# Performance work log

Hardware: AMD Instinct MI355X
Metric: run time of the kernel (lower is better)

The kernel has to match this reference:

```python
import jax, jax.numpy as jnp
import numpy as np
import math

B, T, D = 2, 2048, 2048
H, KV, HD = 16, 4, 128  # n_heads, n_kv_heads, head_dim
ROPE_BASE = 10000.0


def setup_inputs() -> dict:
    key = jax.random.key(0)
    ks = jax.random.split(key, 5)
    s = 0.02
    return {
        "x": jax.random.normal(ks[0], (B, T, D), dtype=jnp.float32),
        "Wq": jax.random.normal(ks[1], (D, H * HD), dtype=jnp.float32) * s,
        "Wk": jax.random.normal(ks[2], (D, KV * HD), dtype=jnp.float32) * s,
        "Wv": jax.random.normal(ks[3], (D, KV * HD), dtype=jnp.float32) * s,
        "Wo": jax.random.normal(ks[4], (H * HD, D), dtype=jnp.float32) * s,
    }


def _rope_tables(t_len, dtype):
    inv_freq = 1.0 / (ROPE_BASE ** (jnp.arange(0, HD, 2, dtype=jnp.float32) / HD))
    t = jnp.arange(t_len, dtype=jnp.float32)
    freqs = t[:, None] * inv_freq[None, :]  # [T, HD/2]
    return jnp.cos(freqs).astype(dtype), jnp.sin(freqs).astype(dtype)


def _apply_rope(x, cos, sin):
    # x: [B, h, T, HD]; cos/sin: [T, HD/2] broadcast to [1,1,T,HD/2]
    c = cos[None, None, :, :]
    s = sin[None, None, :, :]
    x1, x2 = x[..., ::2], x[..., 1::2]
    rot = jnp.stack([x1 * c - x2 * s, x1 * s + x2 * c], axis=-1)  # interleave back
    return rot.reshape(x.shape)


def reference(x, Wq, Wk, Wv, Wo):
    b, t, d = x.shape
    q = (x @ Wq).reshape(b, t, H, HD).transpose(0, 2, 1, 3)   # [B,H,T,HD]
    k = (x @ Wk).reshape(b, t, KV, HD).transpose(0, 2, 1, 3)  # [B,KV,T,HD]
    v = (x @ Wv).reshape(b, t, KV, HD).transpose(0, 2, 1, 3)

    cos, sin = _rope_tables(t, x.dtype)
    q = _apply_rope(q, cos, sin)
    k = _apply_rope(k, cos, sin)

    rep = H // KV
    k_rep = jnp.repeat(k, rep, axis=1)  # [B,H,T,HD]
    v_rep = jnp.repeat(v, rep, axis=1)

    scale = 1.0 / math.sqrt(HD)
    scores = jnp.einsum("bhqd,bhkd->bhqk", q, k_rep) * scale
    causal = jnp.triu(jnp.ones((t, t), dtype=bool), k=1)
    neg = jnp.finfo(scores.dtype).min
    scores = jnp.where(causal[None, None, :, :], neg, scores)
    attn = jax.nn.softmax(scores, axis=-1)
    out = jnp.einsum("bhqk,bhkd->bhqd", attn, v_rep)
    y = out.transpose(0, 2, 1, 3).reshape(b, t, H * HD) @ Wo
    return y
```

## Files before the change

kernel.cpp:

```cpp
#include <hip/hip_runtime.h>
#include <cstdint>
#include <math.h>

#define T_SEQ 2048
#define BATCH 2
#define NH 16
#define NKV 4
#define HD 128

typedef __attribute__((ext_vector_type(8))) short short8;
typedef __attribute__((ext_vector_type(4))) float f32x4;

__device__ __forceinline__ ushort f2bf(float f) {
  uint32_t u = __builtin_bit_cast(uint32_t, f);
  u += 0x7FFF + ((u >> 16) & 1);
  return (ushort)(u >> 16);
}
__device__ __forceinline__ ushort f2bf_trunc(float f) {
  return (ushort)(__builtin_bit_cast(uint32_t, f) >> 16);
}
__device__ __forceinline__ float bf2f(ushort u) {
  uint32_t v = ((uint32_t)u) << 16;
  return __builtin_bit_cast(float, v);
}
__device__ __forceinline__ void ld16(void* lds, const void* g) {
  __builtin_amdgcn_global_load_lds((const __attribute__((address_space(1))) void*)g,
                                   (__attribute__((address_space(3))) void*)lds,
                                   16, 0, 0);
}

__global__ __launch_bounds__(256) void prep(
    const float* __restrict__ x, ushort* __restrict__ xb,
    const float* __restrict__ Wq, const float* __restrict__ Wk,
    const float* __restrict__ Wv, const float* __restrict__ Wo,
    ushort* __restrict__ wqkvT, ushort* __restrict__ woT) {
  __shared__ float tile[32][33];
  const int bid = blockIdx.x;
  const int tid = threadIdx.x;
  if (bid < 8192) {
    int i = (bid * 256 + tid) * 4;
    float4 v = *(const float4*)&x[i];
    ushort4 o;
    o.x = f2bf(v.x); o.y = f2bf(v.y); o.z = f2bf(v.z); o.w = f2bf(v.w);
    *(ushort4*)&xb[i] = o;
    return;
  }
  const float* in;
  ushort* out;
  int N, lid;
  if (bid < 12288)      { in = Wq; out = wqkvT;                        N = 2048; lid = bid - 8192; }
  else if (bid < 13312) { in = Wk; out = wqkvT + (size_t)2048 * 2048;  N = 512;  lid = bid - 12288; }
  else if (bid < 14336) { in = Wv; out = wqkvT + (size_t)2560 * 2048;  N = 512;  lid = bid - 13312; }
  else                  { in = Wo; out = woT;                          N = 2048; lid = bid - 14336; }
  const int K = 2048;
  const int nb = N / 32;
  const int n0 = (lid % nb) * 32, k0 = (lid / nb) * 32;
  const int r = tid >> 3, c4 = (tid & 7) << 2;
  float4 v = *(const float4*)&in[(size_t)(k0 + r) * N + n0 + c4];
  tile[r][c4 + 0] = v.x; tile[r][c4 + 1] = v.y;
  tile[r][c4 + 2] = v.z; tile[r][c4 + 3] = v.w;
  __syncthreads();
  ushort4 o;
  o.x = f2bf(tile[c4 + 0][r]); o.y = f2bf(tile[c4 + 1][r]);
  o.z = f2bf(tile[c4 + 2][r]); o.w = f2bf(tile[c4 + 3][r]);
  *(ushort4*)&out[(size_t)(n0 + r) * K + k0 + c4] = o;
}

template <typename OutT>
__global__ __launch_bounds__(256) void gemm_bt(const ushort* __restrict__ A,
                                               const ushort* __restrict__ Bt,
                                               OutT* __restrict__ C,
                                               int M, int N, int K) {
  __shared__ __align__(16) ushort As[128 * 32];
  __shared__ __align__(16) ushort Bs[128 * 32];
  const int tid = threadIdx.x;
  const int w = tid >> 6, l = tid & 63;
  const int wr = w >> 1, wc = w & 1;
  const int quad = l >> 4, l15 = l & 15;
  const int bm = blockIdx.y * 128, bn = blockIdx.x * 128;

  f32x4 acc[4][4];
#pragma unroll
  for (int mi = 0; mi < 4; ++mi)
#pragma unroll
    for (int ni = 0; ni < 4; ++ni)
#pragma unroll
      for (int r = 0; r < 4; ++r) acc[mi][ni][r] = 0.f;

  for (int k0 = 0; k0 < K; k0 += 32) {
    __syncthreads();
#pragma unroll
    for (int j = 0; j < 2; ++j) {
      int r0 = w * 32 + j * 16;
      int row = r0 + (l >> 2);
      int gc = (l & 3) ^ ((row >> 1) & 3);
      ld16(&As[r0 * 32], &A[(size_t)(bm + row) * K + k0 + gc * 8]);
      ld16(&Bs[r0 * 32], &Bt[(size_t)(bn + row) * K + k0 + gc * 8]);
    }
    __syncthreads();
    short8 af[4], bf[4];
#pragma unroll
    for (int mi = 0; mi < 4; ++mi) {
      int m = wr * 64 + mi * 16 + l15;
      af[mi] = *(const short8*)&As[m * 32 + (quad ^ ((m >> 1) & 3)) * 8];
    }
#pragma unroll
    for (int ni = 0; ni < 4; ++ni) {
      int n = wc * 64 + ni * 16 + l15;
      bf[ni] = *(const short8*)&Bs[n * 32 + (quad ^ ((n >> 1) & 3)) * 8];
    }
#pragma unroll
    for (int mi = 0; mi < 4; ++mi)
#pragma unroll
      for (int ni = 0; ni < 4; ++ni)
        acc[mi][ni] = __builtin_amdgcn_mfma_f32_16x16x32_bf16(af[mi], bf[ni], acc[mi][ni], 0, 0, 0);
  }
#pragma unroll
  for (int mi = 0; mi < 4; ++mi)
#pragma unroll
    for (int ni = 0; ni < 4; ++ni)
#pragma unroll
      for (int r = 0; r < 4; ++r) {
        int grow = bm + wr * 64 + mi * 16 + quad * 4 + r;
        int gcol = bn + wc * 64 + ni * 16 + l15;
        if constexpr (__is_same(OutT, ushort))
          C[(size_t)grow * N + gcol] = f2bf(acc[mi][ni][r]);
        else
          C[(size_t)grow * N + gcol] = acc[mi][ni][r];
      }
}

__global__ __launch_bounds__(256) void rope_k_bf16(ushort* __restrict__ qkv) {
  int idx = blockIdx.x * 256 + threadIdx.x;
  const int PAIRS_PER_ROW = 256;
  if (idx >= BATCH * T_SEQ * PAIRS_PER_ROW) return;
  int row = idx >> 8;
  int kp = idx & 255;
  int t = row & (T_SEQ - 1);
  int i = kp & 63;
  ushort* ptr = qkv + (size_t)row * 3072 + 2048 + 2 * kp;
  float inv = expf((float)i * -0.14391156831212788f);
  float ang = (float)t * inv;
  float sn, cs;
  sincosf(ang, &sn, &cs);
  float x1 = bf2f(ptr[0]), x2 = bf2f(ptr[1]);
  ptr[0] = f2bf(x1 * cs - x2 * sn);
  ptr[1] = f2bf(x1 * sn + x2 * cs);
}

__global__ __launch_bounds__(256) void transpose_v(const ushort* __restrict__ qkv,
                                                   ushort* __restrict__ vT) {
  __shared__ ushort tile[32][34];
  int m0 = blockIdx.x * 32, d0 = blockIdx.y * 32;
  int r = threadIdx.x >> 3, c4 = (threadIdx.x & 7) << 2;
  ushort4 v = *(const ushort4*)&qkv[(size_t)(m0 + r) * 3072 + 2560 + d0 + c4];
  tile[r][c4 + 0] = v.x; tile[r][c4 + 1] = v.y;
  tile[r][c4 + 2] = v.z; tile[r][c4 + 3] = v.w;
  __syncthreads();
  ushort4 o;
  o.x = tile[c4 + 0][r]; o.y = tile[c4 + 1][r];
  o.z = tile[c4 + 2][r]; o.w = tile[c4 + 3][r];
  *(ushort4*)&vT[(size_t)(d0 + r) * 4096 + m0 + c4] = o;
}

__global__ __launch_bounds__(512, 2) void attn_mfma(const ushort* __restrict__ qkv,
                                                    const ushort* __restrict__ vT,
                                                    ushort* __restrict__ ao) {
  __shared__ __align__(16) ushort Ks[2][64 * 128];
  __shared__ __align__(16) ushort Vt[2][128 * 64];
  __shared__ __align__(16) ushort Ps[8][16 * 64];
  const int tid = threadIdx.x;
  const int w = tid >> 6, l = tid & 63;
  const int quad = l >> 4, l15 = l & 15;
  const int hw = w >> 1, sub = w & 1;
  const int kvh = blockIdx.y, b = blockIdx.z;
  const int h = kvh * 4 + hw;
  const size_t krow0 = (size_t)b * T_SEQ;
  const float SC = 0.12751744595764253f;

  ushort* pw = Ps[w];
  const int within = l & 7;
  const int colbase = l15 >> 3;

  auto stage = [&](int kt, int bufi) {
    const int kt0 = kt << 6;
    ushort* kb = Ks[bufi];
    ushort* vb = Vt[bufi];
#pragma unroll
    for (int j = 0; j < 2; ++j) {
      int r0 = w * 8 + j * 4;
      int row = r0 + (l >> 4);
      int gc = (l & 15) ^ ((row >> 1) & 7);
      ld16(&kb[r0 * 128], &qkv[(krow0 + kt0 + row) * 3072 + 2048 + kvh * 128 + gc * 8]);
    }
#pragma unroll
    for (int j = 0; j < 2; ++j) {
      int r0 = w * 16 + j * 8;
      int row = r0 + (l >> 3);
      int gc = (l & 7) ^ (row & 7);
      ld16(&vb[r0 * 64], &vT[(size_t)(kvh * 128 + row) * 4096 + krow0 + kt0 + gc * 8]);
    }
  };

#pragma unroll 1
  for (int ph = 0; ph < 2; ++ph) {
    const int qt = ph ? (int)blockIdx.x : 63 - (int)blockIdx.x;
    const int qt0 = qt << 5;
    const size_t qrow0 = krow0 + qt0;

    const int t_pos = qt0 + sub * 16 + l15;
    short8 qf[4];
#pragma unroll
    for (int kc = 0; kc < 4; ++kc) {
      short8 raw = *(const short8*)&qkv[(qrow0 + sub * 16 + l15) * 3072 + h * 128 + kc * 32 + quad * 8];
#pragma unroll
      for (int u = 0; u < 4; ++u) {
        int i_idx = kc * 16 + quad * 4 + u;
        float inv = expf((float)i_idx * -0.14391156831212788f);
        float sn, cs;
        sincosf((float)t_pos * inv, &sn, &cs);
        cs *= SC; sn *= SC;
        float x1 = bf2f((ushort)raw[2 * u]);
        float x2 = bf2f((ushort)raw[2 * u + 1]);
        qf[kc][2 * u]     = (short)f2bf(x1 * cs - x2 * sn);
        qf[kc][2 * u + 1] = (short)f2bf(x1 * sn + x2 * cs);
      }
    }

    f32x4 oacc[8];
#pragma unroll
    for (int i = 0; i < 8; ++i)
#pragma unroll
      for (int r = 0; r < 4; ++r) oacc[i][r] = 0.f;
    float lpart[4] = {0.f, 0.f, 0.f, 0.f};

    const int nkt = (qt >> 1) + 1;
    __syncthreads();
    stage(0, 0);
    for (int kt = 0; kt < nkt; ++kt) {
      __syncthreads();
      if (kt + 1 < nkt) stage(kt + 1, (kt + 1) & 1);
      const ushort* kb = Ks[kt & 1];
      const ushort* vb = Vt[kt & 1];

      f32x4 sacc[4];
#pragma unroll
      for (int ni = 0; ni < 4; ++ni)
#pragma unroll
        for (int r = 0; r < 4; ++r) sacc[ni][r] = 0.f;
#pragma unroll
      for (int kc = 0; kc < 4; ++kc) {
#pragma unroll
        for (int ni = 0; ni < 4; ++ni) {
          int n = ni * 16 + l15;
          short8 bfr = *(const short8*)&kb[n * 128 + ((kc * 4 + quad) ^ ((n >> 1) & 7)) * 8];
          sacc[ni] = __builtin_amdgcn_mfma_f32_16x16x32_bf16(qf[kc], bfr, sacc[ni], 0, 0, 0);
        }
      }

      const int kt0 = kt << 6;
      if (kt == nkt - 1) {
        const int rowg = qt0 + sub * 16 + quad * 4;
#pragma unroll
        for (int ni = 0; ni < 4; ++ni) {
          const int colid = kt0 + ni * 16 + l15;
#pragma unroll
          for (int r = 0; r < 4; ++r) {
            float s = (colid > rowg + r) ? -1e30f : sacc[ni][r];
            float pv = __builtin_amdgcn_exp2f(s);
            lpart[r] += pv;
            int prow = quad * 4 + r;
            pw[prow * 64 + (((ni * 2 + colbase) ^ (prow & 7)) << 3) + within] = f2bf_trunc(pv);
          }
        }
      } else {
#pragma unroll
        for (int ni = 0; ni < 4; ++ni)
#pragma unroll
          for (int r = 0; r < 4; ++r) {
            float pv = __builtin_amdgcn_exp2f(sacc[ni][r]);
            lpart[r] += pv;
            int prow = quad * 4 + r;
            pw[prow * 64 + (((ni * 2 + colbase) ^ (prow & 7)) << 3) + within] = f2bf_trunc(pv);
          }
      }

#pragma unroll
      for (int kc = 0; kc < 2; ++kc) {
        short8 a = *(const short8*)&pw[l15 * 64 + ((kc * 4 + quad) ^ (l15 & 7)) * 8];
#pragma unroll
        for (int ni2 = 0; ni2 < 8; ++ni2) {
          int d = ni2 * 16 + l15;
          short8 bfr = *(const short8*)&vb[d * 64 + ((kc * 4 + quad) ^ (d & 7)) * 8];
          oacc[ni2] = __builtin_amdgcn_mfma_f32_16x16x32_bf16(a, bfr, oacc[ni2], 0, 0, 0);
        }
      }
    }

#pragma unroll
    for (int r = 0; r < 4; ++r) {
      float lv = lpart[r];
      lv += __shfl_xor(lv, 1);
      lv += __shfl_xor(lv, 2);
      lv += __shfl_xor(lv, 4);
      lv += __shfl_xor(lv, 8);
      float inv = 1.f / lv;
      size_t grow = qrow0 + sub * 16 + quad * 4 + r;
#pragma unroll
      for (int ni2 = 0; ni2 < 8; ++ni2)
        ao[grow * 2048 + h * 128 + ni2 * 16 + l15] = f2bf(oacc[ni2][r] * inv);
    }
  }
}

extern "C" void kernel_launch(void* const* d_in, const int* in_sizes, int n_in,
                              void* d_out, int out_size, void* d_ws, size_t ws_size,
                              hipStream_t stream) {
  const float* x  = (const float*)d_in[0];
  const float* Wq = (const float*)d_in[1];
  const float* Wk = (const float*)d_in[2];
  const float* Wv = (const float*)d_in[3];
  const float* Wo = (const float*)d_in[4];
  float* y = (float*)d_out;

  const int M = BATCH * T_SEQ;
  ushort* xb    = (ushort*)d_ws;
  ushort* wqkvT = xb + (size_t)M * 2048;
  ushort* woT   = wqkvT + (size_t)3072 * 2048;
  ushort* qkv   = woT + (size_t)2048 * 2048;
  ushort* vTb   = qkv + (size_t)M * 3072;
  ushort* aob   = vTb + (size_t)512 * 4096;

  prep<<<18432, 256, 0, stream>>>(x, xb, Wq, Wk, Wv, Wo, wqkvT, woT);

  gemm_bt<ushort><<<dim3(3072 / 128, M / 128), 256, 0, stream>>>(
      xb, wqkvT, qkv, M, 3072, 2048);

  rope_k_bf16<<<(M * 256 + 255) / 256, 256, 0, stream>>>(qkv);
  transpose_v<<<dim3(M / 32, 512 / 32), 256, 0, stream>>>(qkv, vTb);

  attn_mfma<<<dim3(32, NKV, BATCH), 512, 0, stream>>>(qkv, vTb, aob);

  gemm_bt<float><<<dim3(2048 / 128, M / 128), 256, 0, stream>>>(
      aob, woT, y, M, 2048, 2048);
}
```

Before: 306.6 us.

## Use 256x256-tile 8-wave GEMM with interleaved staging for QKV projection

Adds a new GEMM kernel with 256x256 output tiles, 512 threads and double-buffered LDS. Each K step is split into four phases that interleave global-to-LDS staging with MFMA work, using raw barriers and priority hints. The QKV projection now uses this kernel. Larger tiles raise operand reuse and cut global traffic, but the grid shrinks to 12x16=192 blocks at one block per CU, which may leave CUs idle on a 256-CU device.

Result: slower. 319.7 us (+4.3%).

```diff
diff --git a/kernel.cpp b/kernel.cpp
--- a/kernel.cpp
+++ b/kernel.cpp
@@ -130,6 +130,121 @@
       }
 }
 
+template <typename OutT>
+__global__ __launch_bounds__(512, 1) void gemm_bt256(const ushort* __restrict__ A,
+                                                     const ushort* __restrict__ Bt,
+                                                     OutT* __restrict__ C,
+                                                     int M, int N, int K) {
+  __shared__ __align__(16) ushort As[2][256 * 64];
+  __shared__ __align__(16) ushort Bs[2][256 * 64];
+  const int tid = threadIdx.x;
+  const int w = tid >> 6, l = tid & 63;
+  const int wr = w >> 2, wc = w & 3;
+  const int quad = l >> 4, l15 = l & 15;
+  const int bm = blockIdx.y * 256, bn = blockIdx.x * 256;
+
+  f32x4 acc[8][4];
+#pragma unroll
+  for (int mi = 0; mi < 8; ++mi)
+#pragma unroll
+    for (int ni = 0; ni < 4; ++ni)
+#pragma unroll
+      for (int r = 0; r < 4; ++r) acc[mi][ni][r] = 0.f;
+
+  auto stage_unit = [&](int k0, int buf, int u) {
+    const ushort* __restrict__ src = (u < 2) ? A : Bt;
+    ushort* dst = (u < 2) ? &As[buf][0] : &Bs[buf][0];
+    const int goff = (u < 2) ? bm : bn;
+    const int rb = (u & 1) * 128;
+#pragma unroll
+    for (int j = 0; j < 2; ++j) {
+      int r0 = rb + j * 64 + w * 8;
+      int row = r0 + (l >> 3);
+      int gc = (l & 7) ^ (row & 7);
+      ld16(&dst[r0 * 64], &src[(size_t)(goff + row) * K + k0 + gc * 8]);
+    }
+  };
+
+  short8 af[4][2], bfv[4][2];
+
+#define LOADA8(mh)                                                             \
+  _Pragma("unroll") for (int i = 0; i < 4; ++i) {                              \
+    int m = wr * 128 + ((mh) * 4 + i) * 16 + l15;                              \
+    _Pragma("unroll") for (int ks = 0; ks < 2; ++ks)                           \
+      af[i][ks] = *(const short8*)&as[m * 64 + ((ks * 4 + quad) ^ (m & 7)) * 8]; \
+  }
+#define LOADB4(nf)                                                             \
+  {                                                                            \
+    int n = wc * 64 + (nf) * 16 + l15;                                         \
+    _Pragma("unroll") for (int ks = 0; ks < 2; ++ks)                           \
+      bfv[nf][ks] = *(const short8*)&bs[n * 64 + ((ks * 4 + quad) ^ (n & 7)) * 8]; \
+  }
+#define MFMA16(mh, nh)                                                         \
+  __builtin_amdgcn_s_setprio(1);                                               \
+  _Pragma("unroll") for (int ks = 0; ks < 2; ++ks)                             \
+  _Pragma("unroll") for (int i = 0; i < 4; ++i)                                \
+  _Pragma("unroll") for (int j = 0; j < 2; ++j)                                \
+    acc[(mh) * 4 + i][(nh) * 2 + j] = __builtin_amdgcn_mfma_f32_16x16x32_bf16( \
+        af[i][ks], bfv[(nh) * 2 + j][ks], acc[(mh) * 4 + i][(nh) * 2 + j],     \
+        0, 0, 0);                                                              \
+  __builtin_amdgcn_s_setprio(0);
+
+  const int NT = K >> 6;
+#pragma unroll
+  for (int u = 0; u < 4; ++u) stage_unit(0, 0, u);
+
+  for (int kt = 0; kt < NT; ++kt) {
+    const int buf = kt & 1;
+    const int nk0 = (kt + 1) << 6;
+    const bool pre = (kt + 1 < NT);
+    const ushort* as = &As[buf][0];
+    const ushort* bs = &Bs[buf][0];
+
+    if (pre) {
+      stage_unit(nk0, buf ^ 1, 0);
+      asm volatile("s_waitcnt vmcnt(2)" ::: "memory");
+    } else {
+      asm volatile("s_waitcnt vmcnt(0)" ::: "memory");
+    }
+    asm volatile("s_barrier" ::: "memory");
+    LOADA8(0);
+    LOADB4(0); LOADB4(1);
+    MFMA16(0, 0);
+    asm volatile("s_barrier" ::: "memory");
+
+    if (pre) stage_unit(nk0, buf ^ 1, 1);
+    LOADB4(2); LOADB4(3);
+    MFMA16(0, 1);
+    asm volatile("s_barrier" ::: "memory");
+
+    if (pre) stage_unit(nk0, buf ^ 1, 2);
+    LOADA8(1);
+    MFMA16(1, 1);
+    asm volatile("s_barrier" ::: "memory");
+
+    if (pre) stage_unit(nk0, buf ^ 1, 3);
+    MFMA16(1, 0);
+    asm volatile("s_barrier" ::: "memory");
+  }
+#undef LOADA8
+#undef LOADB4
+#undef MFMA16
+
+#pragma unroll
+  for (int mi = 0; mi < 8; ++mi)
+#pragma unroll
+    for (int ni = 0; ni < 4; ++ni)
+#pragma unroll
+      for (int r = 0; r < 4; ++r) {
+        int grow = bm + wr * 128 + mi * 16 + quad * 4 + r;
+        int gcol = bn + wc * 64 + ni * 16 + l15;
+        if constexpr (__is_same(OutT, ushort))
+          C[(size_t)grow * N + gcol] = f2bf(acc[mi][ni][r]);
+        else
+          C[(size_t)grow * N + gcol] = acc[mi][ni][r];
+      }
+}
+
 __global__ __launch_bounds__(256) void rope_k_bf16(ushort* __restrict__ qkv) {
   int idx = blockIdx.x * 256 + threadIdx.x;
   const int PAIRS_PER_ROW = 256;
@@ -333,7 +448,7 @@
 
   prep<<<18432, 256, 0, stream>>>(x, xb, Wq, Wk, Wv, Wo, wqkvT, woT);
 
-  gemm_bt<ushort><<<dim3(3072 / 128, M / 128), 256, 0, stream>>>(
+  gemm_bt256<ushort><<<dim3(3072 / 256, M / 256), 512, 0, stream>>>(
       xb, wqkvT, qkv, M, 3072, 2048);
 
   rope_k_bf16<<<(M * 256 + 255) / 256, 256, 0, stream>>>(qkv);
```
